# Kernel tuning notes

Hardware: AMD Instinct MI355X
Metric: run time of the kernel (lower is better)

The kernel has to match this reference:

```python
import jax, jax.numpy as jnp
import numpy as np

B, S, D_IN = 2, 2048, 2048
D_OUT, H, RD, L = 2048, 16, 64, 512
HD = D_OUT // H  # 128
ROPE_BASE = 10000.0
EPS = 1e-6


def _rmsnorm(x, w):
    # RMSNorm over last dim
    ms = jnp.mean(jnp.square(x), axis=-1, keepdims=True)
    return x * jax.lax.rsqrt(ms + EPS) * w


def _apply_rope(x, offset):
    # x: [B, H, T, RD]; GPT-NeoX style rotary embedding
    T, rd = x.shape[-2], x.shape[-1]
    pos = (offset + jnp.arange(T)).astype(jnp.float32)  # [T]
    inv_freq = 1.0 / (ROPE_BASE ** (jnp.arange(0, rd, 2, dtype=jnp.float32) / rd))  # [rd/2]
    ang = pos[:, None] * inv_freq[None, :]              # [T, rd/2]
    cos = jnp.cos(jnp.concatenate([ang, ang], axis=-1))  # [T, rd]
    sin = jnp.sin(jnp.concatenate([ang, ang], axis=-1))
    x1, x2 = jnp.split(x, 2, axis=-1)
    rot = jnp.concatenate([-x2, x1], axis=-1)
    return x * cos + rot * sin


def setup_inputs() -> dict:
    key = jax.random.key(0)
    ks = jax.random.split(key, 8)
    sc = 0.02
    return {
        "x": jax.random.normal(ks[0], (B, S, D_IN), jnp.float32),
        "W_DKV": jax.random.normal(ks[1], (L, D_IN), jnp.float32) * sc,
        "W_KRope": jax.random.normal(ks[2], (H * RD, D_IN), jnp.float32) * sc,
        "W_Q": jax.random.normal(ks[3], (D_OUT + H * RD, D_IN), jnp.float32) * sc,
        "W_UK": jax.random.normal(ks[4], (D_OUT, L), jnp.float32) * sc,
        "W_UV": jax.random.normal(ks[5], (D_OUT, L), jnp.float32) * sc,
        "W_O": jax.random.normal(ks[6], (D_IN, D_OUT), jnp.float32) * sc,
        "kv_norm_w": jnp.ones((L,), jnp.float32),
        "offset": 0,
    }


def reference(x, W_DKV, W_KRope, W_Q, W_UK, W_UV, W_O, kv_norm_w, offset):
    b, s, _ = x.shape
    # compressed latent KV (shared across heads)
    c_kv = _rmsnorm(x @ W_DKV.T, kv_norm_w)                      # [B,S,L]
    k_rope = (x @ W_KRope.T).reshape(b, s, H, RD).transpose(0, 2, 1, 3)  # [B,H,S,RD]
    # eval path: fused query projection
    q_total = x @ W_Q.T                                          # [B,S,D_OUT+H*RD]
    q_content = q_total[..., :D_OUT].reshape(b, s, H, HD).transpose(0, 2, 1, 3)  # [B,H,S,HD]
    q_rope = q_total[..., D_OUT:].reshape(b, s, H, RD).transpose(0, 2, 1, 3)     # [B,H,S,RD]
    q_rope = _apply_rope(q_rope, offset)
    k_rope = _apply_rope(k_rope, offset)
    # absorb W_UK into query: q_abs[b,h,s,l]
    w_uk = W_UK.reshape(H, HD, L)
    q_abs = jnp.einsum('bhsd,hdl->bhsl', q_content, w_uk)
    # attention scores against the shared latent + per-head rope keys
    scores = (jnp.einsum('bhsl,btl->bhst', q_abs, c_kv)
              + jnp.einsum('bhsr,bhtr->bhst', q_rope, k_rope))
    scores = scores * jax.lax.rsqrt(jnp.float32(HD + RD))
    t = c_kv.shape[1]
    causal = jnp.arange(t)[None, :] > (jnp.arange(s)[:, None] + offset)  # [S,T]
    scores = jnp.where(causal[None, None], -jnp.inf, scores)
    attn = jax.nn.softmax(scores, axis=-1)                       # [B,H,S,T]
    # attend in latent space, then absorb W_UV on the way out
    ctx_lat = jnp.einsum('bhst,btl->bhsl', attn, c_kv)           # [B,H,S,L]
    w_uv = W_UV.reshape(H, HD, L)
    ctx = jnp.einsum('bhsl,hdl->bhsd', ctx_lat, w_uv)            # [B,H,S,HD]
    ctx = ctx.transpose(0, 2, 1, 3).reshape(b, s, D_OUT)
    return ctx @ W_O.T
```

## Files before the change

kernel.cpp:

```cpp
#include <hip/hip_runtime.h>
#include <hip/hip_bf16.h>
#include <math.h>

#define B_    2
#define S_    2048
#define DIN   2048
#define DOUT  2048
#define H_    16
#define RD_   64
#define L_    512
#define HD_   128
#define BS_   (B_*S_)

typedef __attribute__((ext_vector_type(8))) short bf16x8;
typedef __attribute__((ext_vector_type(4))) float f32x4;

__device__ __forceinline__ short f2bs(float f) {
    __hip_bfloat16 h = __float2bfloat16(f);
    return *reinterpret_cast<short*>(&h);
}
__device__ __forceinline__ float bs2f(short s) {
    unsigned u = ((unsigned)(unsigned short)s) << 16;
    return __uint_as_float(u);
}

__device__ __forceinline__ void gld16(const void* g, void* l) {
    __builtin_amdgcn_global_load_lds(
        (const __attribute__((address_space(1))) unsigned int*)g,
        (__attribute__((address_space(3))) unsigned int*)l, 16, 0, 0);
}

__global__ __launch_bounds__(256) void cast_bf(const float* __restrict__ in,
                                               short* __restrict__ out, int n8)
{
    int i = blockIdx.x * 256 + threadIdx.x;
    if (i >= n8) return;
    float4 a = ((const float4*)in)[i*2], b = ((const float4*)in)[i*2+1];
    bf16x8 t;
    t[0]=f2bs(a.x); t[1]=f2bs(a.y); t[2]=f2bs(a.z); t[3]=f2bs(a.w);
    t[4]=f2bs(b.x); t[5]=f2bs(b.y); t[6]=f2bs(b.z); t[7]=f2bs(b.w);
    ((bf16x8*)out)[i] = t;
}

__global__ __launch_bounds__(256, 4) void gemm_bf(
    const short* __restrict__ A, const short* __restrict__ Bw,
    float* __restrict__ Cf, short* __restrict__ Cb, int N, int K)
{
    __shared__ short As[128*32];
    __shared__ short Bs[128*32];
    const int tid = threadIdx.x;
    const int m0 = blockIdx.y << 7, n0 = blockIdx.x << 7;
    const int w = tid >> 6, lane = tid & 63;
    const int quad = lane >> 4, n16 = lane & 15;
    const int mw = (w & 1) << 6, nw = (w >> 1) << 6;
    const int lr = lane >> 2, cg = lane & 3;
    const int swr = (quad ^ (n16 & 3)) << 3;

    f32x4 acc[4][4];
    #pragma unroll
    for (int mt = 0; mt < 4; mt++)
        #pragma unroll
        for (int nt = 0; nt < 4; nt++) acc[mt][nt] = (f32x4){0.f,0.f,0.f,0.f};

    for (int k0 = 0; k0 < K; k0 += 32) {
        #pragma unroll
        for (int jj = 0; jj < 2; jj++) {
            int rb = (jj*4 + w)*16;
            int r = rb + lr;
            int sc = (cg ^ (r & 3)) << 3;
            gld16(A  + (long long)(m0 + r)*K + k0 + sc, (void*)(As + rb*32));
            gld16(Bw + (long long)(n0 + r)*K + k0 + sc, (void*)(Bs + rb*32));
        }
        __syncthreads();
        bf16x8 af[4], bfr[4];
        #pragma unroll
        for (int t = 0; t < 4; t++) {
            af[t]  = *(const bf16x8*)(As + (mw + t*16 + n16)*32 + swr);
            bfr[t] = *(const bf16x8*)(Bs + (nw + t*16 + n16)*32 + swr);
        }
        #pragma unroll
        for (int mt = 0; mt < 4; mt++)
            #pragma unroll
            for (int nt = 0; nt < 4; nt++)
                acc[mt][nt] = __builtin_amdgcn_mfma_f32_16x16x32_bf16(
                                  af[mt], bfr[nt], acc[mt][nt], 0, 0, 0);
        __syncthreads();
    }

    #pragma unroll
    for (int mt = 0; mt < 4; mt++)
        #pragma unroll
        for (int nt = 0; nt < 4; nt++)
            #pragma unroll
            for (int r = 0; r < 4; r++) {
                long long row = m0 + mw + mt*16 + quad*4 + r;
                int col = n0 + nw + nt*16 + n16;
                if (Cf) Cf[row*(long long)N + col] = acc[mt][nt][r];
                else    Cb[row*(long long)N + col] = f2bs(acc[mt][nt][r]);
            }
}

__global__ __launch_bounds__(256) void rmsnorm_bf(const float* __restrict__ ckv,
                                                  const float* __restrict__ w,
                                                  short* __restrict__ out)
{
    const int row = blockIdx.x;
    const int tid = threadIdx.x;
    const float* p = ckv + (long long)row * L_;
    float v0 = p[tid], v1 = p[tid + 256];
    float ss = v0 * v0 + v1 * v1;
    #pragma unroll
    for (int o = 32; o >= 1; o >>= 1) ss += __shfl_xor(ss, o);
    __shared__ float wsum[4];
    if ((tid & 63) == 0) wsum[tid >> 6] = ss;
    __syncthreads();
    float tot = wsum[0] + wsum[1] + wsum[2] + wsum[3];
    float scale = rsqrtf(tot * (1.0f / (float)L_) + 1e-6f);
    out[(long long)row * L_ + tid]       = f2bs(v0 * scale * w[tid]);
    out[(long long)row * L_ + tid + 256] = f2bs(v1 * scale * w[tid + 256]);
}

__global__ __launch_bounds__(256) void rope_kernel(short* __restrict__ q_bf,
                                                   short* __restrict__ kr_bf,
                                                   const int* __restrict__ offp)
{
    const int offset = offp[0];
    long long idx = (long long)blockIdx.x * 256 + threadIdx.x;
    int r = (int)(idx & 31);
    long long t = idx >> 5;
    int h = (int)(t % H_);
    long long m = t / H_;
    int s = (int)(m % S_);

    float inv = (float)exp(-9.210340371976184 * ((double)r / 32.0));
    float ang = (float)(offset + s) * inv;
    float sn, cs;
    sincosf(ang, &sn, &cs);

    short* q = q_bf + m * 3072 + DOUT + h * RD_;
    float x1 = bs2f(q[r]), x2 = bs2f(q[r + 32]);
    q[r]      = f2bs(x1 * cs - x2 * sn);
    q[r + 32] = f2bs(x2 * cs + x1 * sn);

    short* kk = kr_bf + m * (H_ * RD_) + h * RD_;
    x1 = bs2f(kk[r]); x2 = bs2f(kk[r + 32]);
    kk[r]      = f2bs(x1 * cs - x2 * sn);
    kk[r + 32] = f2bs(x2 * cs + x1 * sn);
}

#define TKC0 0
#define TKR0 16384
#define TVT0 24576
#define TPP0 40960

__global__ __launch_bounds__(512)
__attribute__((amdgpu_waves_per_eu(2, 2)))
void flash_mha(
    const short* __restrict__ q_bf,
    const short* __restrict__ K_up,
    const short* __restrict__ kr_bf,
    const short* __restrict__ V_upT,
    const int* __restrict__ offp,
    short* __restrict__ ctx_bf)
{
    __shared__ short lds[50176];
    const int offset = offp[0];
    const int bh = blockIdx.y;
    const int b = bh >> 4, h = bh & 15;
    const int r0 = (int)(gridDim.x - 1 - blockIdx.x) * 128;
    const int tid = threadIdx.x;
    const int w = tid >> 6, lane = tid & 63;
    const int quad = lane >> 4, n16 = lane & 15;
    const int rx3 = (n16 & 7) << 3;
    const float scale = rsqrtf((float)(HD_ + RD_));

    const int l4 = lane >> 4, g16 = lane & 15;
    const int l8 = lane >> 3, g8 = lane & 7;

    const short* kc_src = K_up  + ((long long)b*S_)*2048 + h*HD_;
    const short* kr_src = kr_bf + ((long long)b*S_)*1024 + h*RD_;
    const short* vt_src = V_upT + ((long long)(b*S_ + h*HD_))*2048;

    auto stage = [&](int tk, int bf) {
        #pragma unroll
        for (int j = 0; j < 2; j++) {
            int r4 = (w*2 + j)*4;
            int row = r4 + l4;
            int gs = g16 ^ (row & 7);
            gld16(kc_src + (long long)(tk + row)*2048 + gs*8,
                  (void*)(lds + TKC0 + bf*8192 + r4*128));
        }
        {
            int row = w*8 + l8;
            int gs = g8 ^ (l8 & 7);
            gld16(kr_src + (long long)(tk + row)*1024 + gs*8,
                  (void*)(lds + TKR0 + bf*4096 + w*512));
        }
        #pragma unroll
        for (int j = 0; j < 2; j++) {
            int d8 = (w*2 + j)*8;
            int d = d8 + l8;
            int gs = g8 ^ (l8 & 7);
            gld16(vt_src + (long long)d*2048 + tk + gs*8,
                  (void*)(lds + TVT0 + bf*8192 + d8*64));
        }
    };

    stage(0, 0);

    bf16x8 qf[6];
    {
        const short* qp = q_bf + ((long long)(b*S_ + r0 + w*16 + n16))*3072;
        #pragma unroll
        for (int ks = 0; ks < 4; ks++)
            qf[ks] = *(const bf16x8*)(qp + h*HD_ + ks*32 + quad*8);
        #pragma unroll
        for (int ks = 0; ks < 2; ks++)
            qf[4+ks] = *(const bf16x8*)(qp + DOUT + h*RD_ + ks*32 + quad*8);
    }

    f32x4 Oacc[8];
    #pragma unroll
    for (int v = 0; v < 8; v++) Oacc[v] = (f32x4){0.f,0.f,0.f,0.f};
    float mrun[4] = {-INFINITY,-INFINITY,-INFINITY,-INFINITY};
    float lrun[4] = {0.f,0.f,0.f,0.f};

    int tmax = r0 + 128 + offset;
    if (tmax > S_) tmax = S_;

    for (int t0 = 0, bf = 0; t0 < tmax; t0 += 64, bf ^= 1) {
        asm volatile("s_waitcnt vmcnt(0)" ::: "memory");
        __builtin_amdgcn_s_barrier();
        __builtin_amdgcn_sched_barrier(0);

        if (t0 + 64 < tmax) stage(t0 + 64, bf ^ 1);

        const short* kcb = lds + TKC0 + bf*8192;
        const short* krb = lds + TKR0 + bf*4096;
        f32x4 Sf[4];
        #pragma unroll
        for (int nt = 0; nt < 4; nt++) {
            f32x4 a = {0.f,0.f,0.f,0.f};
            const short* kc = kcb + (nt*16 + n16)*128;
            #pragma unroll
            for (int ks = 0; ks < 4; ks++)
                a = __builtin_amdgcn_mfma_f32_16x16x32_bf16(
                        qf[ks], *(const bf16x8*)(kc + ((ks*32 + quad*8) ^ rx3)),
                        a, 0, 0, 0);
            const short* kr = krb + (nt*16 + n16)*64;
            a = __builtin_amdgcn_mfma_f32_16x16x32_bf16(
                    qf[4], *(const bf16x8*)(kr + ((quad*8) ^ rx3)), a, 0, 0, 0);
            a = __builtin_amdgcn_mfma_f32_16x16x32_bf16(
                    qf[5], *(const bf16x8*)(kr + ((32 + quad*8) ^ rx3)), a, 0, 0, 0);
            Sf[nt] = a;
        }

        float e0[4][4], lm[4];
        #pragma unroll
        for (int r = 0; r < 4; r++) {
            const int srow = r0 + w*16 + quad*4 + r;
            lm[r] = -INFINITY;
            #pragma unroll
            for (int nt = 0; nt < 4; nt++) {
                int t = t0 + nt*16 + n16;
                float s = (t <= srow + offset) ? Sf[nt][r]*scale : -INFINITY;
                e0[r][nt] = s;
                lm[r] = fmaxf(lm[r], s);
            }
        }
        bool trig = (lm[0] > mrun[0] + 8.f) | (lm[1] > mrun[1] + 8.f)
                  | (lm[2] > mrun[2] + 8.f) | (lm[3] > mrun[3] + 8.f);
        if (__any((int)trig)) {
            float al[4];
            #pragma unroll
            for (int r = 0; r < 4; r++) {
                float tm = lm[r];
                tm = fmaxf(tm, __shfl_xor(tm, 1));
                tm = fmaxf(tm, __shfl_xor(tm, 2));
                tm = fmaxf(tm, __shfl_xor(tm, 4));
                tm = fmaxf(tm, __shfl_xor(tm, 8));
                if (tm > mrun[r]) { al[r] = __expf(mrun[r] - tm); mrun[r] = tm; }
                else al[r] = 1.f;
            }
            #pragma unroll
            for (int v = 0; v < 8; v++) {
                Oacc[v][0] *= al[0]; Oacc[v][1] *= al[1];
                Oacc[v][2] *= al[2]; Oacc[v][3] *= al[3];
            }
            lrun[0] *= al[0]; lrun[1] *= al[1];
            lrun[2] *= al[2]; lrun[3] *= al[3];
        }
        #pragma unroll
        for (int r = 0; r < 4; r++) {
            float ps = 0.f;
            #pragma unroll
            for (int nt = 0; nt < 4; nt++) {
                float ex = __expf(e0[r][nt] - mrun[r]);
                ps += ex;
                lds[TPP0 + w*1152 + (quad*4 + r)*72 + nt*16 + n16] = f2bs(ex);
            }
            lrun[r] += ps;
        }

        const short* vtb = lds + TVT0 + bf*8192;
        bf16x8 pf0 = *(const bf16x8*)(lds + TPP0 + w*1152 + n16*72 + quad*8);
        bf16x8 pf1 = *(const bf16x8*)(lds + TPP0 + w*1152 + n16*72 + 32 + quad*8);
        const int vo0 = (quad*8) ^ rx3, vo1 = (32 + quad*8) ^ rx3;
        #pragma unroll
        for (int v = 0; v < 8; v++) {
            const short* vb = vtb + (v*16 + n16)*64;
            Oacc[v] = __builtin_amdgcn_mfma_f32_16x16x32_bf16(
                          pf0, *(const bf16x8*)(vb + vo0), Oacc[v], 0, 0, 0);
            Oacc[v] = __builtin_amdgcn_mfma_f32_16x16x32_bf16(
                          pf1, *(const bf16x8*)(vb + vo1), Oacc[v], 0, 0, 0);
        }
    }

    float inv[4];
    #pragma unroll
    for (int r = 0; r < 4; r++) {
        float s = lrun[r];
        s += __shfl_xor(s, 1);
        s += __shfl_xor(s, 2);
        s += __shfl_xor(s, 4);
        s += __shfl_xor(s, 8);
        inv[r] = 1.0f / s;
    }
    #pragma unroll
    for (int v = 0; v < 8; v++)
        #pragma unroll
        for (int r = 0; r < 4; r++) {
            long long row = (long long)b*S_ + r0 + w*16 + quad*4 + r;
            ctx_bf[row*2048 + h*HD_ + v*16 + n16] = f2bs(Oacc[v][r]*inv[r]);
        }
}

extern "C" void kernel_launch(void* const* d_in, const int* in_sizes, int n_in,
                              void* d_out, int out_size, void* d_ws, size_t ws_size,
                              hipStream_t stream)
{
    const float* x       = (const float*)d_in[0];
    const float* W_DKV   = (const float*)d_in[1];
    const float* W_KRope = (const float*)d_in[2];
    const float* W_Q     = (const float*)d_in[3];
    const float* W_UK    = (const float*)d_in[4];
    const float* W_UV    = (const float*)d_in[5];
    const float* W_O     = (const float*)d_in[6];
    const float* kvnw    = (const float*)d_in[7];
    const int*   offp    = (const int*)d_in[8];
    float* out = (float*)d_out;

    float* ws = (float*)d_ws;
    float* c_kv    = ws;
    short* x_bf    = (short*)(c_kv + 2097152);
    short* q_bf    = x_bf    + 8388608;
    short* kr_bf   = q_bf    + 12582912;
    short* c_kv_bf = kr_bf   + 4194304;
    short* wuk_bf  = c_kv_bf + 2097152;
    short* wuv_bf  = wuk_bf  + 1048576;
    short* wdkv_bf = wuv_bf  + 1048576;
    short* wkr_bf  = wdkv_bf + 1048576;
    short* wq_bf   = wkr_bf  + 2097152;
    short* wo_bf   = wq_bf   + 6291456;
    short* ctx_bf  = wo_bf   + 4194304;
    short* V_upT   = ctx_bf  + 8388608;
    short* K_up    = x_bf;

    dim3 blk(256);

    cast_bf<<<4096, blk, 0, stream>>>(x, x_bf, 1048576);
    cast_bf<<<512,  blk, 0, stream>>>(W_DKV, wdkv_bf, 131072);
    cast_bf<<<1024, blk, 0, stream>>>(W_KRope, wkr_bf, 262144);
    cast_bf<<<3072, blk, 0, stream>>>(W_Q, wq_bf, 786432);
    cast_bf<<<2048, blk, 0, stream>>>(W_O, wo_bf, 524288);
    cast_bf<<<512,  blk, 0, stream>>>(W_UK, wuk_bf, 131072);
    cast_bf<<<512,  blk, 0, stream>>>(W_UV, wuv_bf, 131072);

    gemm_bf<<<dim3(3072/128, 32), blk, 0, stream>>>(
        x_bf, wq_bf, nullptr, q_bf, 3072, 2048);
    gemm_bf<<<dim3(1024/128, 32), blk, 0, stream>>>(
        x_bf, wkr_bf, nullptr, kr_bf, 1024, 2048);
    gemm_bf<<<dim3(512/128, 32), blk, 0, stream>>>(
        x_bf, wdkv_bf, c_kv, nullptr, 512, 2048);
    rmsnorm_bf<<<4096, blk, 0, stream>>>(c_kv, kvnw, c_kv_bf);

    gemm_bf<<<dim3(2048/128, 32), blk, 0, stream>>>(
        c_kv_bf, wuk_bf, nullptr, K_up, 2048, 512);
    gemm_bf<<<dim3(2048/128, 16), blk, 0, stream>>>(
        wuv_bf, c_kv_bf, nullptr, V_upT, 2048, 512);
    gemm_bf<<<dim3(2048/128, 16), blk, 0, stream>>>(
        wuv_bf, c_kv_bf + (long long)S_*512, nullptr,
        V_upT + (long long)S_*2048, 2048, 512);

    rope_kernel<<<8192, blk, 0, stream>>>(q_bf, kr_bf, offp);

    flash_mha<<<dim3(S_/128, B_*H_), dim3(512), 0, stream>>>(
        q_bf, K_up, kr_bf, V_upT, offp, ctx_bf);

    gemm_bf<<<dim3(2048/128, 32), blk, 0, stream>>>(
        ctx_bf, wo_bf, out, nullptr, 2048, 2048);
}
```

Measured before the change: 528.5 us.

## Fuse casts and Q/KRope GEMMs, batch V GEMM, triple-buffer attention K/V staging

All seven fp32-to-bf16 casts become one launch, and W_Q and W_KRope are concatenated so a single GEMM produces Q, q_rope and k_rope into a 4096-wide buffer. The two V_upT GEMMs become one batched launch through a new z-dimension stride. The flash attention kernel moves from double to triple buffering in LDS with a partial vmcnt wait, so two tiles are in flight during compute. RoPE uses a float __expf in place of double exp. The larger LDS footprint may reduce occupancy, and the fast exp slightly changes precision.

```diff
diff --git a/kernel.cpp b/kernel.cpp
--- a/kernel.cpp
+++ b/kernel.cpp
@@ -30,22 +30,41 @@
         (__attribute__((address_space(3))) unsigned int*)l, 16, 0, 0);
 }
 
-__global__ __launch_bounds__(256) void cast_bf(const float* __restrict__ in,
-                                               short* __restrict__ out, int n8)
-{
-    int i = blockIdx.x * 256 + threadIdx.x;
-    if (i >= n8) return;
-    float4 a = ((const float4*)in)[i*2], b = ((const float4*)in)[i*2+1];
+__global__ __launch_bounds__(256) void cast_all(
+    const float* __restrict__ x,    const float* __restrict__ wq,
+    const float* __restrict__ wkr,  const float* __restrict__ wdkv,
+    const float* __restrict__ wo,   const float* __restrict__ wuk,
+    const float* __restrict__ wuv,
+    short* __restrict__ x_bf,   short* __restrict__ wqkr_bf,
+    short* __restrict__ wdkv_bf, short* __restrict__ wo_bf,
+    short* __restrict__ wuk_bf,  short* __restrict__ wuv_bf)
+{
+    long long i = (long long)blockIdx.x * 256 + threadIdx.x;
+    const float* src; short* dst; long long off;
+    if      (i < 1048576) { src = x;    dst = x_bf;              off = i; }
+    else if (i < 1835008) { src = wq;   dst = wqkr_bf;           off = i - 1048576; }
+    else if (i < 2097152) { src = wkr;  dst = wqkr_bf + 6291456; off = i - 1835008; }
+    else if (i < 2228224) { src = wdkv; dst = wdkv_bf;           off = i - 2097152; }
+    else if (i < 2752512) { src = wo;   dst = wo_bf;             off = i - 2228224; }
+    else if (i < 2883584) { src = wuk;  dst = wuk_bf;            off = i - 2752512; }
+    else                  { src = wuv;  dst = wuv_bf;            off = i - 2883584; }
+    float4 a = ((const float4*)src)[off*2], b = ((const float4*)src)[off*2+1];
     bf16x8 t;
     t[0]=f2bs(a.x); t[1]=f2bs(a.y); t[2]=f2bs(a.z); t[3]=f2bs(a.w);
     t[4]=f2bs(b.x); t[5]=f2bs(b.y); t[6]=f2bs(b.z); t[7]=f2bs(b.w);
-    ((bf16x8*)out)[i] = t;
+    ((bf16x8*)dst)[off] = t;
 }
 
 __global__ __launch_bounds__(256, 4) void gemm_bf(
     const short* __restrict__ A, const short* __restrict__ Bw,
-    float* __restrict__ Cf, short* __restrict__ Cb, int N, int K)
-{
+    float* __restrict__ Cf, short* __restrict__ Cb, int N, int K,
+    long long az, long long bz, long long cz)
+{
+    const int z = blockIdx.z;
+    A  += (long long)z * az;
+    Bw += (long long)z * bz;
+    if (Cf) Cf += (long long)z * cz; else Cb += (long long)z * cz;
+
     __shared__ short As[128*32];
     __shared__ short Bs[128*32];
     const int tid = threadIdx.x;
@@ -120,8 +139,7 @@
     out[(long long)row * L_ + tid + 256] = f2bs(v1 * scale * w[tid + 256]);
 }
 
-__global__ __launch_bounds__(256) void rope_kernel(short* __restrict__ q_bf,
-                                                   short* __restrict__ kr_bf,
+__global__ __launch_bounds__(256) void rope_kernel(short* __restrict__ qkr,
                                                    const int* __restrict__ offp)
 {
     const int offset = offp[0];
@@ -132,38 +150,35 @@
     long long m = t / H_;
     int s = (int)(m % S_);
 
-    float inv = (float)exp(-9.210340371976184 * ((double)r / 32.0));
+    float inv = __expf(-0.28782314f * (float)r);
     float ang = (float)(offset + s) * inv;
     float sn, cs;
     sincosf(ang, &sn, &cs);
 
-    short* q = q_bf + m * 3072 + DOUT + h * RD_;
+    short* q = qkr + m * 4096 + 2048 + h * RD_;
     float x1 = bs2f(q[r]), x2 = bs2f(q[r + 32]);
     q[r]      = f2bs(x1 * cs - x2 * sn);
     q[r + 32] = f2bs(x2 * cs + x1 * sn);
 
-    short* kk = kr_bf + m * (H_ * RD_) + h * RD_;
+    short* kk = qkr + m * 4096 + 3072 + h * RD_;
     x1 = bs2f(kk[r]); x2 = bs2f(kk[r + 32]);
     kk[r]      = f2bs(x1 * cs - x2 * sn);
     kk[r + 32] = f2bs(x2 * cs + x1 * sn);
 }
 
-#define TKC0 0
-#define TKR0 16384
-#define TVT0 24576
-#define TPP0 40960
+#define SBUF 20480
+#define TPP0 61440
 
 __global__ __launch_bounds__(512)
 __attribute__((amdgpu_waves_per_eu(2, 2)))
 void flash_mha(
-    const short* __restrict__ q_bf,
+    const short* __restrict__ qkr,
     const short* __restrict__ K_up,
-    const short* __restrict__ kr_bf,
     const short* __restrict__ V_upT,
     const int* __restrict__ offp,
     short* __restrict__ ctx_bf)
 {
-    __shared__ short lds[50176];
+    __shared__ short lds[70656];
     const int offset = offp[0];
     const int bh = blockIdx.y;
     const int b = bh >> 4, h = bh & 15;
@@ -178,23 +193,24 @@
     const int l8 = lane >> 3, g8 = lane & 7;
 
     const short* kc_src = K_up  + ((long long)b*S_)*2048 + h*HD_;
-    const short* kr_src = kr_bf + ((long long)b*S_)*1024 + h*RD_;
+    const short* kr_src = qkr   + ((long long)b*S_)*4096 + 3072 + h*RD_;
     const short* vt_src = V_upT + ((long long)(b*S_ + h*HD_))*2048;
 
-    auto stage = [&](int tk, int bf) {
+    auto stage = [&](int tk, int bi) {
+        short* base = lds + bi*SBUF;
         #pragma unroll
         for (int j = 0; j < 2; j++) {
             int r4 = (w*2 + j)*4;
             int row = r4 + l4;
             int gs = g16 ^ (row & 7);
             gld16(kc_src + (long long)(tk + row)*2048 + gs*8,
-                  (void*)(lds + TKC0 + bf*8192 + r4*128));
+                  (void*)(base + r4*128));
         }
         {
             int row = w*8 + l8;
             int gs = g8 ^ (l8 & 7);
-            gld16(kr_src + (long long)(tk + row)*1024 + gs*8,
-                  (void*)(lds + TKR0 + bf*4096 + w*512));
+            gld16(kr_src + (long long)(tk + row)*4096 + gs*8,
+                  (void*)(base + 8192 + w*512));
         }
         #pragma unroll
         for (int j = 0; j < 2; j++) {
@@ -202,22 +218,25 @@
             int d = d8 + l8;
             int gs = g8 ^ (l8 & 7);
             gld16(vt_src + (long long)d*2048 + tk + gs*8,
-                  (void*)(lds + TVT0 + bf*8192 + d8*64));
+                  (void*)(base + 12288 + d8*64));
         }
     };
-
-    stage(0, 0);
 
     bf16x8 qf[6];
     {
-        const short* qp = q_bf + ((long long)(b*S_ + r0 + w*16 + n16))*3072;
+        const short* qp = qkr + ((long long)(b*S_ + r0 + w*16 + n16))*4096;
         #pragma unroll
         for (int ks = 0; ks < 4; ks++)
             qf[ks] = *(const bf16x8*)(qp + h*HD_ + ks*32 + quad*8);
-        #pragma unroll
-        for (int ks = 0; ks < 2; ks++)
-            qf[4+ks] = *(const bf16x8*)(qp + DOUT + h*RD_ + ks*32 + quad*8);
+        qf[4] = *(const bf16x8*)(qp + 2048 + h*RD_ + quad*8);
+        qf[5] = *(const bf16x8*)(qp + 2048 + h*RD_ + 32 + quad*8);
     }
+
+    int tmax = r0 + 128 + offset;
+    if (tmax > S_) tmax = S_;
+
+    stage(0, 0);
+    stage(64, 1);
 
     f32x4 Oacc[8];
     #pragma unroll
@@ -225,18 +244,22 @@
     float mrun[4] = {-INFINITY,-INFINITY,-INFINITY,-INFINITY};
     float lrun[4] = {0.f,0.f,0.f,0.f};
 
-    int tmax = r0 + 128 + offset;
-    if (tmax > S_) tmax = S_;
-
-    for (int t0 = 0, bf = 0; t0 < tmax; t0 += 64, bf ^= 1) {
-        asm volatile("s_waitcnt vmcnt(0)" ::: "memory");
+    int bi = 0;
+    for (int t0 = 0; t0 < tmax; t0 += 64) {
+        if (t0 + 64 < tmax) asm volatile("s_waitcnt vmcnt(5)" ::: "memory");
+        else                asm volatile("s_waitcnt vmcnt(0)" ::: "memory");
         __builtin_amdgcn_s_barrier();
         __builtin_amdgcn_sched_barrier(0);
 
-        if (t0 + 64 < tmax) stage(t0 + 64, bf ^ 1);
-
-        const short* kcb = lds + TKC0 + bf*8192;
-        const short* krb = lds + TKR0 + bf*4096;
+        {
+            int bi2 = bi + 2; if (bi2 >= 3) bi2 -= 3;
+            if (t0 + 128 < tmax) stage(t0 + 128, bi2);
+        }
+
+        const short* kcb = lds + bi*SBUF;
+        const short* krb = kcb + 8192;
+        const short* vtb = kcb + 12288;
+
         f32x4 Sf[4];
         #pragma unroll
         for (int nt = 0; nt < 4; nt++) {
@@ -302,7 +325,6 @@
             lrun[r] += ps;
         }
 
-        const short* vtb = lds + TVT0 + bf*8192;
         bf16x8 pf0 = *(const bf16x8*)(lds + TPP0 + w*1152 + n16*72 + quad*8);
         bf16x8 pf1 = *(const bf16x8*)(lds + TPP0 + w*1152 + n16*72 + 32 + quad*8);
         const int vo0 = (quad*8) ^ rx3, vo1 = (32 + quad*8) ^ rx3;
@@ -314,6 +336,8 @@
             Oacc[v] = __builtin_amdgcn_mfma_f32_16x16x32_bf16(
                           pf1, *(const bf16x8*)(vb + vo1), Oacc[v], 0, 0, 0);
         }
+
+        bi = bi + 1; if (bi >= 3) bi = 0;
     }
 
     float inv[4];
@@ -353,50 +377,40 @@
     float* ws = (float*)d_ws;
     float* c_kv    = ws;
     short* x_bf    = (short*)(c_kv + 2097152);
-    short* q_bf    = x_bf    + 8388608;
-    short* kr_bf   = q_bf    + 12582912;
-    short* c_kv_bf = kr_bf   + 4194304;
+    short* qkr_bf  = x_bf    + 8388608;
+    short* c_kv_bf = qkr_bf  + 16777216;
     short* wuk_bf  = c_kv_bf + 2097152;
     short* wuv_bf  = wuk_bf  + 1048576;
     short* wdkv_bf = wuv_bf  + 1048576;
-    short* wkr_bf  = wdkv_bf + 1048576;
-    short* wq_bf   = wkr_bf  + 2097152;
-    short* wo_bf   = wq_bf   + 6291456;
+    short* wqkr_bf = wdkv_bf + 1048576;
+    short* wo_bf   = wqkr_bf + 8388608;
     short* ctx_bf  = wo_bf   + 4194304;
     short* V_upT   = ctx_bf  + 8388608;
     short* K_up    = x_bf;
 
     dim3 blk(256);
 
-    cast_bf<<<4096, blk, 0, stream>>>(x, x_bf, 1048576);
-    cast_bf<<<512,  blk, 0, stream>>>(W_DKV, wdkv_bf, 131072);
-    cast_bf<<<1024, blk, 0, stream>>>(W_KRope, wkr_bf, 262144);
-    cast_bf<<<3072, blk, 0, stream>>>(W_Q, wq_bf, 786432);
-    cast_bf<<<2048, blk, 0, stream>>>(W_O, wo_bf, 524288);
-    cast_bf<<<512,  blk, 0, stream>>>(W_UK, wuk_bf, 131072);
-    cast_bf<<<512,  blk, 0, stream>>>(W_UV, wuv_bf, 131072);
-
-    gemm_bf<<<dim3(3072/128, 32), blk, 0, stream>>>(
-        x_bf, wq_bf, nullptr, q_bf, 3072, 2048);
-    gemm_bf<<<dim3(1024/128, 32), blk, 0, stream>>>(
-        x_bf, wkr_bf, nullptr, kr_bf, 1024, 2048);
-    gemm_bf<<<dim3(512/128, 32), blk, 0, stream>>>(
-        x_bf, wdkv_bf, c_kv, nullptr, 512, 2048);
+    cast_all<<<11776, blk, 0, stream>>>(
+        x, W_Q, W_KRope, W_DKV, W_O, W_UK, W_UV,
+        x_bf, wqkr_bf, wdkv_bf, wo_bf, wuk_bf, wuv_bf);
+
+    gemm_bf<<<dim3(32, 32), blk, 0, stream>>>(
+        x_bf, wqkr_bf, nullptr, qkr_bf, 4096, 2048, 0, 0, 0);
+    gemm_bf<<<dim3(4, 32), blk, 0, stream>>>(
+        x_bf, wdkv_bf, c_kv, nullptr, 512, 2048, 0, 0, 0);
     rmsnorm_bf<<<4096, blk, 0, stream>>>(c_kv, kvnw, c_kv_bf);
 
-    gemm_bf<<<dim3(2048/128, 32), blk, 0, stream>>>(
-        c_kv_bf, wuk_bf, nullptr, K_up, 2048, 512);
-    gemm_bf<<<dim3(2048/128, 16), blk, 0, stream>>>(
-        wuv_bf, c_kv_bf, nullptr, V_upT, 2048, 512);
-    gemm_bf<<<dim3(2048/128, 16), blk, 0, stream>>>(
-        wuv_bf, c_kv_bf + (long long)S_*512, nullptr,
-        V_upT + (long long)S_*2048, 2048, 512);
-
-    rope_kernel<<<8192, blk, 0, stream>>>(q_bf, kr_bf, offp);
+    gemm_bf<<<dim3(16, 32), blk, 0, stream>>>(
+        c_kv_bf, wuk_bf, nullptr, K_up, 2048, 512, 0, 0, 0);
+    gemm_bf<<<dim3(16, 16, 2), blk, 0, stream>>>(
+        wuv_bf, c_kv_bf, nullptr, V_upT, 2048, 512,
+        0, (long long)S_*512, (long long)S_*2048);
+
+    rope_kernel<<<8192, blk, 0, stream>>>(qkr_bf, offp);
 
     flash_mha<<<dim3(S_/128, B_*H_), dim3(512), 0, stream>>>(
-        q_bf, K_up, kr_bf, V_upT, offp, ctx_bf);
-
-    gemm_bf<<<dim3(2048/128, 32), blk, 0, stream>>>(
-        ctx_bf, wo_bf, out, nullptr, 2048, 2048);
-}
+        qkr_bf, K_up, V_upT, offp, ctx_bf);
+
+    gemm_bf<<<dim3(16, 32), blk, 0, stream>>>(
+        ctx_bf, wo_bf, out, nullptr, 2048, 2048, 0, 0, 0);
+}
```

After: 474.9 us. -10.2%, faster.
